# Optimization experiments

Measured on AMD Instinct MI355X. Metric: run time of the kernel, lower is better.

Reference implementation:

```python
import jax, jax.numpy as jnp
import numpy as np
import math

N_NODES = 100000
N_EDGES = 600000
HIDDEN = 128
HEADS = 8
HEAD_DIM = HIDDEN // HEADS
TEMPORAL = 32


def _xavier(key, fan_in, fan_out):
    bound = math.sqrt(6.0 / (fan_in + fan_out))
    return jax.random.uniform(key, (fan_in, fan_out), jnp.float32, -bound, bound)


def setup_inputs() -> dict:
    key = jax.random.key(0)
    ks = jax.random.split(key, 16)
    inp = {
        'query': jax.random.normal(ks[0], (N_NODES, HIDDEN), jnp.float32),
        'key': jax.random.normal(ks[1], (N_NODES, HIDDEN), jnp.float32),
        'value': jax.random.normal(ks[2], (N_NODES, HIDDEN), jnp.float32),
        'temporal_encoding': jax.random.normal(ks[3], (N_EDGES, TEMPORAL), jnp.float32),
        'edge_index': jax.random.randint(ks[4], (2, N_EDGES), 0, N_NODES, jnp.int64),
        # projection weights stored as [in, out] so y = x @ W + b
        'Wq': _xavier(ks[5], HIDDEN, HIDDEN), 'bq': jnp.zeros((HIDDEN,), jnp.float32),
        'Wk': _xavier(ks[6], HIDDEN, HIDDEN), 'bk': jnp.zeros((HIDDEN,), jnp.float32),
        'Wv': _xavier(ks[7], HIDDEN, HIDDEN), 'bv': jnp.zeros((HIDDEN,), jnp.float32),
        'Wtq': _xavier(ks[8], TEMPORAL, HIDDEN), 'btq': jnp.zeros((HIDDEN,), jnp.float32),
        'Wtk': _xavier(ks[9], TEMPORAL, HIDDEN), 'btk': jnp.zeros((HIDDEN,), jnp.float32),
        'Wout': _xavier(ks[10], HIDDEN, HIDDEN), 'bout': jnp.zeros((HIDDEN,), jnp.float32),
    }
    return inp


def reference(query, key, value, temporal_encoding, edge_index,
              Wq, bq, Wk, bk, Wv, bv, Wtq, btq, Wtk, btk, Wout, bout):
    n = query.shape[0]
    H, hd = HEADS, HEAD_DIM
    Q = (query @ Wq + bq).reshape(n, H, hd)
    K = (key @ Wk + bk).reshape(n, H, hd)
    V = (value @ Wv + bv).reshape(n, H, hd)
    tq = (temporal_encoding @ Wtq + btq).reshape(-1, H, hd)
    tk = (temporal_encoding @ Wtk + btk).reshape(-1, H, hd)

    src, tgt = edge_index[0], edge_index[1]
    # per-edge, per-head scores [E, H]
    scores = jnp.sum(Q[src] * K[tgt], axis=-1) / math.sqrt(hd)
    scores = scores + jnp.sum(tq * tk, axis=-1)

    # segment softmax over edges grouped by target node (stable, per head)
    seg_max = jax.ops.segment_max(scores, tgt, num_segments=n)  # [N, H]
    e = jnp.exp(scores - seg_max[tgt])
    seg_sum = jax.ops.segment_sum(e, tgt, num_segments=n)       # [N, H]
    attn_weights = e / seg_sum[tgt]                              # [E, H]

    # weighted scatter-add aggregation of source values onto targets
    agg = jax.ops.segment_sum(attn_weights[..., None] * V[src], tgt, num_segments=n)  # [N, H, hd]
    attn_output = agg.reshape(n, HIDDEN) @ Wout + bout
    return attn_output, attn_weights
```

## Files before the change

### kernel.cpp

```cpp
#include <hip/hip_runtime.h>
#include <hip/hip_bf16.h>

#define HID 128
#define MAXD 64
#define TBLK 512

typedef __attribute__((ext_vector_type(8))) short bfrag8;
typedef __attribute__((ext_vector_type(4))) short bf4;
typedef __attribute__((ext_vector_type(4))) float facc4;

__device__ inline short f2bf(float x) {
  unsigned u = __builtin_bit_cast(unsigned, x);
  u += 0x7fffu + ((u >> 16) & 1u);
  return (short)(u >> 16);
}
__device__ inline float bf2f(short s) {
  unsigned u = ((unsigned)(unsigned short)s) << 16;
  return __builtin_bit_cast(float, u);
}

__global__ __launch_bounds__(256) void init_k(
    const float* __restrict__ Wq, const float* __restrict__ Wk,
    const float* __restrict__ Wv, const float* __restrict__ Wout,
    const float* __restrict__ Wtq, const float* __restrict__ Wtk,
    short* __restrict__ out, int* __restrict__ degcur, int n2) {
  int gid = blockIdx.x * 256 + threadIdx.x;
  if (gid < n2) degcur[gid] = 0;
  if (gid >= 9216) return;
  bfrag8 v;
  if (gid < 8192) {
    int which = gid >> 11;
    int chunk = gid & 2047;
    const float* W = (which == 0) ? Wq : (which == 1) ? Wk
                   : (which == 2) ? Wv : Wout;
    int c  = chunk & 15;
    int g  = (chunk >> 4) & 3;
    int kt = (chunk >> 6) & 3;
    int ct = chunk >> 8;
    int col = ct * 16 + c;
    int k0 = kt * 32 + g * 8;
    #pragma unroll
    for (int i = 0; i < 8; ++i) v[i] = f2bf(W[(size_t)(k0 + i) * HID + col]);
  } else {
    int chunk = gid - 8192;
    int c  = chunk & 15;
    int g  = (chunk >> 4) & 3;
    int ct = (chunk >> 6) & 7;
    int qk = chunk >> 9;
    const float* W = qk ? Wtk : Wtq;
    int col = ct * 16 + c;
    int k0 = g * 8;
    #pragma unroll
    for (int i = 0; i < 8; ++i) v[i] = f2bf(W[(size_t)(k0 + i) * HID + col]);
  }
  *(bfrag8*)(out + (size_t)gid * 8) = v;
}

template <typename IT, typename OT, int MODE>
__device__ __forceinline__ void gemm_body(
    short* __restrict__ Ws, float* __restrict__ bshf, short* __restrict__ Xs,
    const IT* __restrict__ X, const short* __restrict__ Wp,
    const float* __restrict__ b, OT* __restrict__ Y, int nrows, int ch) {
  const int t = threadIdx.x;
  #pragma unroll
  for (int it = 0; it < 4; ++it) {
    int chunk = t + it * 512;
    *(bfrag8*)(&Ws[chunk * 8]) = *(const bfrag8*)(Wp + (size_t)chunk * 8);
  }
  if (t < 128) bshf[t] = b[t];
  if constexpr (sizeof(IT) == 4) {
    int row = t >> 3;
    int arow = min(ch * 64 + row, nrows - 1);
    const float* xp = (const float*)X + (size_t)arow * HID + (t & 7) * 16;
    float xv[16];
    *(facc4*)(xv)      = *(const facc4*)(xp);
    *(facc4*)(xv + 4)  = *(const facc4*)(xp + 4);
    *(facc4*)(xv + 8)  = *(const facc4*)(xp + 8);
    *(facc4*)(xv + 12) = *(const facc4*)(xp + 12);
    bfrag8 p0, p1;
    #pragma unroll
    for (int i = 0; i < 8; ++i) { p0[i] = f2bf(xv[i]); p1[i] = f2bf(xv[8 + i]); }
    int u0 = (t & 7) * 2;
    *(bfrag8*)(&Xs[row * 128 + ((u0    ) ^ (row & 7)) * 8]) = p0;
    *(bfrag8*)(&Xs[row * 128 + ((u0 + 1) ^ (row & 7)) * 8]) = p1;
  }
  __syncthreads();

  const int w  = t >> 6;
  const int l  = t & 63;
  const int lr = l & 15;
  const int g  = l >> 4;
  const int ctbase = (w >> 2) * 4;
  const int row0 = ch * 64 + (w & 3) * 16;
  const int xr = (w & 3) * 16 + lr;

  facc4 acc[4];
  #pragma unroll
  for (int c2 = 0; c2 < 4; ++c2)
    acc[c2] = *(const facc4*)(&bshf[(ctbase + c2) * 16 + g * 4]);

  #pragma unroll
  for (int kt = 0; kt < 4; ++kt) {
    bfrag8 a;
    if constexpr (sizeof(IT) == 4) {
      a = *(const bfrag8*)(&Xs[xr * 128 + ((kt * 4 + g) ^ (xr & 7)) * 8]);
    } else {
      int arow = min(row0 + lr, nrows - 1);
      a = *(const bfrag8*)((const short*)X + (size_t)arow * HID + kt * 32 + g * 8);
    }
    #pragma unroll
    for (int c2 = 0; c2 < 4; ++c2) {
      int ct = ctbase + c2;
      bfrag8 bf = *(const bfrag8*)(&Ws[(((ct * 4 + kt) * 4 + g) * 16 + lr) * 8]);
      acc[c2] = __builtin_amdgcn_mfma_f32_16x16x32_bf16(bf, a, acc[c2], 0, 0, 0);
    }
  }

  const int row = row0 + lr;
  if (row < nrows) {
    #pragma unroll
    for (int c2 = 0; c2 < 4; ++c2) {
      const int col0 = (ctbase + c2) * 16 + g * 4;
      if constexpr (sizeof(OT) == 4) {
        *(facc4*)((float*)Y + (size_t)row * HID + col0) = acc[c2];
      } else {
        bf4 p;
        #pragma unroll
        for (int j = 0; j < 4; ++j) p[j] = f2bf(acc[c2][j]);
        size_t base;
        if constexpr (MODE == 0) base = (size_t)row * HID + col0;
        else base = (size_t)row * 256 + col0 + (MODE == 2 ? 128 : 0);
        *(bf4*)((short*)Y + base) = p;
      }
    }
  }
}

__device__ __forceinline__ void temporal_body(
    short* __restrict__ Ws, float* __restrict__ bsh, float* __restrict__ tsh,
    short* __restrict__ Ts, const float* __restrict__ T,
    const short* __restrict__ Wp, const float* __restrict__ btq,
    const float* __restrict__ btk, float* __restrict__ ts,
    int E, int ntiles, int bx, int nblk) {
  const int t = threadIdx.x;
  #pragma unroll
  for (int it = 0; it < 2; ++it) {
    int chunk = t + it * 512;
    *(bfrag8*)(&Ws[chunk * 8]) = *(const bfrag8*)(Wp + (size_t)chunk * 8);
  }
  if (t < 256) bsh[t] = (t < 128) ? btq[t] : btk[t - 128];
  __syncthreads();

  const int w = t >> 6;
  const int l = t & 63;
  const int c = l & 15;
  const int g = l >> 4;
  float* mytsh = tsh + w * 160;

  for (int tile = bx; tile < ntiles; tile += nblk) {
    __syncthreads();
    {
      int r = t >> 2;
      int ar = min(tile * 128 + r, E - 1);
      const float* tp = T + (size_t)ar * 32 + (t & 3) * 8;
      float xv[8];
      *(facc4*)(xv)     = *(const facc4*)(tp);
      *(facc4*)(xv + 4) = *(const facc4*)(tp + 4);
      bfrag8 p;
      #pragma unroll
      for (int i = 0; i < 8; ++i) p[i] = f2bf(xv[i]);
      *(bfrag8*)(&Ts[r * 40 + (t & 3) * 8]) = p;
    }
    __syncthreads();

    const int e0 = tile * 128 + w * 16;
    bfrag8 tb = *(const bfrag8*)(&Ts[(w * 16 + c) * 40 + g * 8]);

    #pragma unroll 1
    for (int ct = 0; ct < 8; ++ct) {
      facc4 accq = *(const facc4*)(&bsh[ct * 16 + g * 4]);
      bfrag8 wq = *(const bfrag8*)(&Ws[(ct * 64 + g * 16 + c) * 8]);
      accq = __builtin_amdgcn_mfma_f32_16x16x32_bf16(wq, tb, accq, 0, 0, 0);
      facc4 acck = *(const facc4*)(&bsh[128 + ct * 16 + g * 4]);
      bfrag8 wk = *(const bfrag8*)(&Ws[(512 + ct * 64 + g * 16 + c) * 8]);
      acck = __builtin_amdgcn_mfma_f32_16x16x32_bf16(wk, tb, acck, 0, 0, 0);

      float s = accq[0] * acck[0] + accq[1] * acck[1] +
                accq[2] * acck[2] + accq[3] * acck[3];
      s += __shfl_xor(s, 16, 64);
      s += __shfl_xor(s, 32, 64);
      if (g == 0) mytsh[c * 10 + ct] = s;
    }
    int e = e0 + (l >> 2);
    if (e < E) {
      float2 v2 = *(const float2*)(&mytsh[(l >> 2) * 10 + (l & 3) * 2]);
      *(float2*)(ts + (size_t)e0 * 8 + l * 2) = v2;
    }
  }
}

__global__ __launch_bounds__(512, 6) void mega_k(
    const float* __restrict__ query, const float* __restrict__ key,
    const float* __restrict__ value, const float* __restrict__ temporal,
    const short* __restrict__ Wpre,
    const float* __restrict__ bq, const float* __restrict__ bk,
    const float* __restrict__ bv, const float* __restrict__ btq,
    const float* __restrict__ btk,
    short* __restrict__ QVp, short* __restrict__ Kp,
    float* __restrict__ tscores, const int* __restrict__ tgt,
    int* __restrict__ deg, int N, int E, int nch, int ntiles) {
  __shared__ __align__(16) char smem[49664];
  short* Ws = (short*)smem;
  const int bx = blockIdx.x;
  if (bx < 3 * nch) {
    float* baux = (float*)(smem + 32768);
    short* Xs = (short*)(smem + 33280);
    const int role = bx % 3;
    const int ch = bx / 3;
    if (role == 0)
      gemm_body<float, short, 1>(Ws, baux, Xs, query, Wpre + 0 * 16384, bq, QVp, N, ch);
    else if (role == 1)
      gemm_body<float, short, 0>(Ws, baux, Xs, key, Wpre + 1 * 16384, bk, Kp, N, ch);
    else
      gemm_body<float, short, 2>(Ws, baux, Xs, value, Wpre + 2 * 16384, bv, QVp, N, ch);
  } else if (bx < 3 * nch + TBLK) {
    temporal_body(Ws, (float*)(smem + 16384), (float*)(smem + 17408),
                  (short*)(smem + 23808),
                  temporal, Wpre + 4 * 16384, btq, btk, tscores, E, ntiles,
                  bx - 3 * nch, TBLK);
  } else {
    int gid = (bx - 3 * nch - TBLK) * 512 + threadIdx.x;
    if (gid < E) atomicAdd(&deg[tgt[gid]], 1);
  }
}

template <typename IT, typename OT, int MODE>
__global__ __launch_bounds__(512, 6) void gemm_mfma_k(
    const IT* __restrict__ X, const short* __restrict__ Wp,
    const float* __restrict__ b, OT* __restrict__ Y, int nrows) {
  __shared__ __align__(16) char smem[49664];
  gemm_body<IT, OT, MODE>((short*)smem, (float*)(smem + 32768),
                          (short*)(smem + 33280), X, Wp, b, Y, nrows,
                          blockIdx.x);
}

__global__ __launch_bounds__(256) void block_sum_k(const int* __restrict__ deg,
                                                   int* __restrict__ bsum, int n) {
  __shared__ int sd[256];
  const int base = blockIdx.x * 1024;
  const int t = threadIdx.x;
  int s = 0;
  #pragma unroll
  for (int j = 0; j < 4; ++j) {
    int i = base + t + j * 256;
    if (i < n) s += deg[i];
  }
  sd[t] = s;
  __syncthreads();
  for (int st = 128; st; st >>= 1) {
    if (t < st) sd[t] += sd[t + st];
    __syncthreads();
  }
  if (t == 0) bsum[blockIdx.x] = sd[0];
}

__global__ __launch_bounds__(1024) void scan_partials_k(const int* __restrict__ bsum,
                                                        int* __restrict__ boff, int G) {
  __shared__ int sd[1024];
  const int t = threadIdx.x;
  int v = (t < G) ? bsum[t] : 0;
  sd[t] = v;
  __syncthreads();
  for (int s = 1; s < 1024; s <<= 1) {
    int a = (t >= s) ? sd[t - s] : 0;
    __syncthreads();
    sd[t] += a;
    __syncthreads();
  }
  if (t < G) boff[t] = sd[t] - v;
}

__global__ __launch_bounds__(256) void block_scan_k(const int* __restrict__ deg,
                                                    const int* __restrict__ boff,
                                                    int* __restrict__ off, int n) {
  __shared__ int sd[256];
  const int base = blockIdx.x * 1024;
  const int t = threadIdx.x;
  const int i0 = base + t * 4;
  int v[4];
  int s = 0;
  #pragma unroll
  for (int j = 0; j < 4; ++j) {
    v[j] = (i0 + j < n) ? deg[i0 + j] : 0;
    s += v[j];
  }
  const int own = s;
  sd[t] = s;
  __syncthreads();
  for (int st = 1; st < 256; st <<= 1) {
    int a = (t >= st) ? sd[t - st] : 0;
    __syncthreads();
    sd[t] += a;
    __syncthreads();
  }
  int acc = boff[blockIdx.x] + sd[t] - own;
  #pragma unroll
  for (int j = 0; j < 4; ++j) {
    int idx = i0 + j;
    if (idx < n) {
      off[idx] = acc;
      acc += v[j];
      if (idx == n - 1) off[n] = acc;
    }
  }
}

__global__ __launch_bounds__(256) void scatter_k(const int* __restrict__ src,
                                                 const int* __restrict__ tgt,
                                                 const int* __restrict__ off,
                                                 int* __restrict__ cur,
                                                 int2* __restrict__ elist2, int E) {
  int gid = blockIdx.x * 256 + threadIdx.x;
  if (gid < E) {
    int n = tgt[gid];
    int p = atomicAdd(&cur[n], 1);
    elist2[off[n] + p] = make_int2(gid, src[gid]);
  }
}

__global__ __launch_bounds__(256) void softmax_agg_k(
    const float* __restrict__ tscores, const short* __restrict__ QVp,
    const short* __restrict__ Kp, const int* __restrict__ off,
    const int2* __restrict__ elist2, float* __restrict__ attn_w,
    short* __restrict__ aggb, int N) {
  __shared__ int esh[8][MAXD];
  __shared__ int ssh[8][MAXD];
  __shared__ float sraw[8][MAXD][8];
  const int t = threadIdx.x;
  const int grp = t >> 5;
  const int g = t & 31;
  const int h = g >> 2;
  const int j = g & 3;
  const int n = blockIdx.x * 8 + grp;
  if (n >= N) return;

  const int s0 = off[n];
  const int deg = off[n + 1] - s0;

  float kr[4];
  {
    bf4 k4 = *(const bf4*)(Kp + (size_t)n * HID + g * 4);
    #pragma unroll
    for (int q = 0; q < 4; ++q) kr[q] = bf2f(k4[q]);
  }

  if (deg <= MAXD) {
    for (int i = g; i < deg; i += 32) {
      int2 es = elist2[s0 + i];
      esh[grp][i] = es.x;
      ssh[grp][i] = es.y;
    }

    float lsum = 0.f;
    float a0 = 0.f, a1 = 0.f, a2 = 0.f, a3 = 0.f;
    int i = 0;
    for (; i + 4 <= deg; i += 4) {
      const size_t b0 = (size_t)ssh[grp][i]     * 256 + g * 4;
      const size_t b1 = (size_t)ssh[grp][i + 1] * 256 + g * 4;
      const size_t b2 = (size_t)ssh[grp][i + 2] * 256 + g * 4;
      const size_t b3 = (size_t)ssh[grp][i + 3] * 256 + g * 4;
      bf4 q0 = *(const bf4*)(QVp + b0);
      bf4 q1 = *(const bf4*)(QVp + b1);
      bf4 q2 = *(const bf4*)(QVp + b2);
      bf4 q3 = *(const bf4*)(QVp + b3);
      bf4 v0 = *(const bf4*)(QVp + b0 + 128);
      bf4 v1 = *(const bf4*)(QVp + b1 + 128);
      bf4 v2 = *(const bf4*)(QVp + b2 + 128);
      bf4 v3 = *(const bf4*)(QVp + b3 + 128);
      float ts0 = tscores[(size_t)esh[grp][i]     * 8 + h];
      float ts1 = tscores[(size_t)esh[grp][i + 1] * 8 + h];
      float ts2 = tscores[(size_t)esh[grp][i + 2] * 8 + h];
      float ts3 = tscores[(size_t)esh[grp][i + 3] * 8 + h];
      float p0 = bf2f(q0[0]) * kr[0] + bf2f(q0[1]) * kr[1] +
                 bf2f(q0[2]) * kr[2] + bf2f(q0[3]) * kr[3];
      float p1 = bf2f(q1[0]) * kr[0] + bf2f(q1[1]) * kr[1] +
                 bf2f(q1[2]) * kr[2] + bf2f(q1[3]) * kr[3];
      float p2 = bf2f(q2[0]) * kr[0] + bf2f(q2[1]) * kr[1] +
                 bf2f(q2[2]) * kr[2] + bf2f(q2[3]) * kr[3];
      float p3 = bf2f(q3[0]) * kr[0] + bf2f(q3[1]) * kr[1] +
                 bf2f(q3[2]) * kr[2] + bf2f(q3[3]) * kr[3];
      p0 += __shfl_xor(p0, 1, 4); p0 += __shfl_xor(p0, 2, 4);
      p1 += __shfl_xor(p1, 1, 4); p1 += __shfl_xor(p1, 2, 4);
      p2 += __shfl_xor(p2, 1, 4); p2 += __shfl_xor(p2, 2, 4);
      p3 += __shfl_xor(p3, 1, 4); p3 += __shfl_xor(p3, 2, 4);
      float w0 = __expf(ts0 + p0 * 0.25f);
      float w1 = __expf(ts1 + p1 * 0.25f);
      float w2 = __expf(ts2 + p2 * 0.25f);
      float w3 = __expf(ts3 + p3 * 0.25f);
      if (j == 0) {
        sraw[grp][i][h]     = w0;
        sraw[grp][i + 1][h] = w1;
        sraw[grp][i + 2][h] = w2;
        sraw[grp][i + 3][h] = w3;
      }
      lsum += (w0 + w1) + (w2 + w3);
      a0 += w0 * bf2f(v0[0]) + w1 * bf2f(v1[0]) +
            w2 * bf2f(v2[0]) + w3 * bf2f(v3[0]);
      a1 += w0 * bf2f(v0[1]) + w1 * bf2f(v1[1]) +
            w2 * bf2f(v2[1]) + w3 * bf2f(v3[1]);
      a2 += w0 * bf2f(v0[2]) + w1 * bf2f(v1[2]) +
            w2 * bf2f(v2[2]) + w3 * bf2f(v3[2]);
      a3 += w0 * bf2f(v0[3]) + w1 * bf2f(v1[3]) +
            w2 * bf2f(v2[3]) + w3 * bf2f(v3[3]);
    }
    for (; i < deg; ++i) {
      const size_t b0 = (size_t)ssh[grp][i] * 256 + g * 4;
      bf4 q0 = *(const bf4*)(QVp + b0);
      bf4 v0 = *(const bf4*)(QVp + b0 + 128);
      float ts0 = tscores[(size_t)esh[grp][i] * 8 + h];
      float p0 = bf2f(q0[0]) * kr[0] + bf2f(q0[1]) * kr[1] +
                 bf2f(q0[2]) * kr[2] + bf2f(q0[3]) * kr[3];
      p0 += __shfl_xor(p0, 1, 4); p0 += __shfl_xor(p0, 2, 4);
      float w0 = __expf(ts0 + p0 * 0.25f);
      if (j == 0) sraw[grp][i][h] = w0;
      lsum += w0;
      a0 += w0 * bf2f(v0[0]);
      a1 += w0 * bf2f(v0[1]);
      a2 += w0 * bf2f(v0[2]);
      a3 += w0 * bf2f(v0[3]);
    }
    float invl = (lsum > 0.f) ? 1.0f / lsum : 0.f;

    bf4 st;
    st[0] = f2bf(a0 * invl); st[1] = f2bf(a1 * invl);
    st[2] = f2bf(a2 * invl); st[3] = f2bf(a3 * invl);
    *(bf4*)(aggb + (size_t)n * HID + g * 4) = st;

    if (j == 0) {
      for (int q = 0; q < deg; ++q)
        attn_w[(size_t)esh[grp][q] * 8 + h] = sraw[grp][q][h] * invl;
    }
  } else {
    float m = -3.0e38f;
    for (int q = 0; q < deg; ++q) {
      int2 es = elist2[s0 + q];
      bf4 q4 = *(const bf4*)(QVp + (size_t)es.y * 256 + g * 4);
      float p = bf2f(q4[0]) * kr[0] + bf2f(q4[1]) * kr[1] +
                bf2f(q4[2]) * kr[2] + bf2f(q4[3]) * kr[3];
      p += __shfl_xor(p, 1, 4); p += __shfl_xor(p, 2, 4);
      m = fmaxf(m, tscores[(size_t)es.x * 8 + h] + p * 0.25f);
    }
    float l = 0.f;
    for (int q = 0; q < deg; ++q) {
      int2 es = elist2[s0 + q];
      bf4 q4 = *(const bf4*)(QVp + (size_t)es.y * 256 + g * 4);
      float p = bf2f(q4[0]) * kr[0] + bf2f(q4[1]) * kr[1] +
                bf2f(q4[2]) * kr[2] + bf2f(q4[3]) * kr[3];
      p += __shfl_xor(p, 1, 4); p += __shfl_xor(p, 2, 4);
      l += __expf(tscores[(size_t)es.x * 8 + h] + p * 0.25f - m);
    }
    float invl = (l > 0.f) ? 1.0f / l : 0.f;
    float a0 = 0.f, a1 = 0.f, a2 = 0.f, a3 = 0.f;
    for (int q = 0; q < deg; ++q) {
      int2 es = elist2[s0 + q];
      bf4 q4 = *(const bf4*)(QVp + (size_t)es.y * 256 + g * 4);
      bf4 v4 = *(const bf4*)(QVp + (size_t)es.y * 256 + 128 + g * 4);
      float p = bf2f(q4[0]) * kr[0] + bf2f(q4[1]) * kr[1] +
                bf2f(q4[2]) * kr[2] + bf2f(q4[3]) * kr[3];
      p += __shfl_xor(p, 1, 4); p += __shfl_xor(p, 2, 4);
      float w = __expf(tscores[(size_t)es.x * 8 + h] + p * 0.25f - m) * invl;
      a0 += w * bf2f(v4[0]);
      a1 += w * bf2f(v4[1]);
      a2 += w * bf2f(v4[2]);
      a3 += w * bf2f(v4[3]);
      if (j == 0) attn_w[(size_t)es.x * 8 + h] = w;
    }
    bf4 st;
    st[0] = f2bf(a0); st[1] = f2bf(a1); st[2] = f2bf(a2); st[3] = f2bf(a3);
    *(bf4*)(aggb + (size_t)n * HID + g * 4) = st;
  }
}

extern "C" void kernel_launch(void* const* d_in, const int* in_sizes, int n_in,
                              void* d_out, int out_size, void* d_ws, size_t ws_size,
                              hipStream_t stream) {
  const float* query    = (const float*)d_in[0];
  const float* key      = (const float*)d_in[1];
  const float* value    = (const float*)d_in[2];
  const float* temporal = (const float*)d_in[3];
  const int*   eidx     = (const int*)d_in[4];
  const float* Wq   = (const float*)d_in[5];
  const float* bq   = (const float*)d_in[6];
  const float* Wk   = (const float*)d_in[7];
  const float* bk   = (const float*)d_in[8];
  const float* Wv   = (const float*)d_in[9];
  const float* bv   = (const float*)d_in[10];
  const float* Wtq  = (const float*)d_in[11];
  const float* btq  = (const float*)d_in[12];
  const float* Wtk  = (const float*)d_in[13];
  const float* btk  = (const float*)d_in[14];
  const float* Wout = (const float*)d_in[15];
  const float* bout = (const float*)d_in[16];

  const int N = in_sizes[0] / HID;
  const int E = in_sizes[4] / 2;
  const int* src = eidx;
  const int* tgt = eidx + E;

  char* ws = (char*)d_ws;
  short* QVp = (short*)ws;                     ws += (size_t)N * 256 * 2;
  short* Kp = (short*)ws;                      ws += (size_t)N * HID * 2;
  short* aggb = (short*)ws;                    ws += (size_t)N * HID * 2;
  float* tscores = (float*)ws;                 ws += (size_t)E * 8 * 4;
  int* deg   = (int*)ws;                       ws += (size_t)N * 4;
  int* cur   = (int*)ws;                       ws += (size_t)N * 4;
  int* off   = (int*)ws;                       ws += (size_t)(N + 2) * 4;
  int2* elist2 = (int2*)ws;                    ws += (size_t)E * 8;
  int* bsum  = (int*)ws;                       ws += 1024 * 4;
  int* boff  = (int*)ws;                       ws += 1024 * 4;
  short* Wpre = (short*)ws;

  const int G = (N + 1023) / 1024;
  const int nch = (N + 63) / 64;
  const int ntiles = (E + 127) / 128;
  const int cblk = (E + 511) / 512;

  dim3 b256(256), b512(512);
  init_k<<<(2 * N + 255) / 256, b256, 0, stream>>>(Wq, Wk, Wv, Wout, Wtq, Wtk,
                                                   Wpre, deg, 2 * N);
  mega_k<<<3 * nch + TBLK + cblk, b512, 0, stream>>>(
      query, key, value, temporal, Wpre, bq, bk, bv, btq, btk,
      QVp, Kp, tscores, tgt, deg, N, E, nch, ntiles);

  block_sum_k<<<G, b256, 0, stream>>>(deg, bsum, N);
  scan_partials_k<<<1, 1024, 0, stream>>>(bsum, boff, G);
  block_scan_k<<<G, b256, 0, stream>>>(deg, boff, off, N);
  scatter_k<<<(E + 255) / 256, b256, 0, stream>>>(src, tgt, off, cur, elist2, E);

  float* attn_w = (float*)d_out + (size_t)N * HID;
  softmax_agg_k<<<(N + 7) / 8, b256, 0, stream>>>(tscores, QVp, Kp, off,
                                                  elist2, attn_w, aggb, N);

  gemm_mfma_k<short, float, 0><<<nch, b512, 0, stream>>>(aggb, Wpre + 3 * 16384,
                                                         bout, (float*)d_out, N);
}
```

Before: 223.1 us.

## Fuse three-kernel degree scan into single-pass decoupled look-back scan

```diff
diff --git a/kernel.cpp b/kernel.cpp
--- a/kernel.cpp
+++ b/kernel.cpp
@@ -23,9 +23,9 @@
     const float* __restrict__ Wq, const float* __restrict__ Wk,
     const float* __restrict__ Wv, const float* __restrict__ Wout,
     const float* __restrict__ Wtq, const float* __restrict__ Wtk,
-    short* __restrict__ out, int* __restrict__ degcur, int n2) {
+    short* __restrict__ out, int* __restrict__ zero_base, int nzero) {
   int gid = blockIdx.x * 256 + threadIdx.x;
-  if (gid < n2) degcur[gid] = 0;
+  if (gid < nzero) zero_base[gid] = 0;
   if (gid >= 9216) return;
   bfrag8 v;
   if (gid < 8192) {
@@ -244,47 +244,14 @@
                           blockIdx.x);
 }
 
-__global__ __launch_bounds__(256) void block_sum_k(const int* __restrict__ deg,
-                                                   int* __restrict__ bsum, int n) {
+__global__ __launch_bounds__(256) void scan_fused_k(
+    const int* __restrict__ deg, int* __restrict__ off,
+    int* __restrict__ aggs, int* __restrict__ prefs, int* __restrict__ flags,
+    int n) {
   __shared__ int sd[256];
-  const int base = blockIdx.x * 1024;
-  const int t = threadIdx.x;
-  int s = 0;
-  #pragma unroll
-  for (int j = 0; j < 4; ++j) {
-    int i = base + t + j * 256;
-    if (i < n) s += deg[i];
-  }
-  sd[t] = s;
-  __syncthreads();
-  for (int st = 128; st; st >>= 1) {
-    if (t < st) sd[t] += sd[t + st];
-    __syncthreads();
-  }
-  if (t == 0) bsum[blockIdx.x] = sd[0];
-}
-
-__global__ __launch_bounds__(1024) void scan_partials_k(const int* __restrict__ bsum,
-                                                        int* __restrict__ boff, int G) {
-  __shared__ int sd[1024];
-  const int t = threadIdx.x;
-  int v = (t < G) ? bsum[t] : 0;
-  sd[t] = v;
-  __syncthreads();
-  for (int s = 1; s < 1024; s <<= 1) {
-    int a = (t >= s) ? sd[t - s] : 0;
-    __syncthreads();
-    sd[t] += a;
-    __syncthreads();
-  }
-  if (t < G) boff[t] = sd[t] - v;
-}
-
-__global__ __launch_bounds__(256) void block_scan_k(const int* __restrict__ deg,
-                                                    const int* __restrict__ boff,
-                                                    int* __restrict__ off, int n) {
-  __shared__ int sd[256];
-  const int base = blockIdx.x * 1024;
+  __shared__ int sbase;
+  const int b = blockIdx.x;
+  const int base = b * 1024;
   const int t = threadIdx.x;
   const int i0 = base + t * 4;
   int v[4];
@@ -303,7 +270,25 @@
     sd[t] += a;
     __syncthreads();
   }
-  int acc = boff[blockIdx.x] + sd[t] - own;
+  if (t == 0) {
+    const int total = sd[255];
+    aggs[b] = total;
+    __threadfence();
+    atomicExch(&flags[b], 1);
+    int running = 0;
+    for (int p = b - 1; p >= 0; --p) {
+      int f;
+      do { f = atomicAdd(&flags[p], 0); } while (f == 0);
+      if (f == 2) { running += atomicAdd(&prefs[p], 0); break; }
+      running += atomicAdd(&aggs[p], 0);
+    }
+    prefs[b] = running + total;
+    __threadfence();
+    atomicExch(&flags[b], 2);
+    sbase = running;
+  }
+  __syncthreads();
+  int acc = sbase + sd[t] - own;
   #pragma unroll
   for (int j = 0; j < 4; ++j) {
     int idx = i0 + j;
@@ -514,27 +499,27 @@
   float* tscores = (float*)ws;                 ws += (size_t)E * 8 * 4;
   int* deg   = (int*)ws;                       ws += (size_t)N * 4;
   int* cur   = (int*)ws;                       ws += (size_t)N * 4;
+  int* flags = (int*)ws;                       ws += 1024 * 4;
   int* off   = (int*)ws;                       ws += (size_t)(N + 2) * 4;
   int2* elist2 = (int2*)ws;                    ws += (size_t)E * 8;
-  int* bsum  = (int*)ws;                       ws += 1024 * 4;
-  int* boff  = (int*)ws;                       ws += 1024 * 4;
+  int* aggs  = (int*)ws;                       ws += 1024 * 4;
+  int* prefs = (int*)ws;                       ws += 1024 * 4;
   short* Wpre = (short*)ws;
 
   const int G = (N + 1023) / 1024;
   const int nch = (N + 63) / 64;
   const int ntiles = (E + 127) / 128;
   const int cblk = (E + 511) / 512;
+  const int nzero = 2 * N + 1024;
 
   dim3 b256(256), b512(512);
-  init_k<<<(2 * N + 255) / 256, b256, 0, stream>>>(Wq, Wk, Wv, Wout, Wtq, Wtk,
-                                                   Wpre, deg, 2 * N);
+  init_k<<<(nzero + 255) / 256, b256, 0, stream>>>(Wq, Wk, Wv, Wout, Wtq, Wtk,
+                                                   Wpre, deg, nzero);
   mega_k<<<3 * nch + TBLK + cblk, b512, 0, stream>>>(
       query, key, value, temporal, Wpre, bq, bk, bv, btq, btk,
       QVp, Kp, tscores, tgt, deg, N, E, nch, ntiles);
 
-  block_sum_k<<<G, b256, 0, stream>>>(deg, bsum, N);
-  scan_partials_k<<<1, 1024, 0, stream>>>(bsum, boff, G);
-  block_scan_k<<<G, b256, 0, stream>>>(deg, boff, off, N);
+  scan_fused_k<<<G, b256, 0, stream>>>(deg, off, aggs, prefs, flags, N);
   scatter_k<<<(E + 255) / 256, b256, 0, stream>>>(src, tgt, off, cur, elist2, E);
 
   float* attn_w = (float*)d_out + (size_t)N * HID;
```

New measurement: 229.5 us. +2.9%, slower.
